# Kernel tuning notes

Hardware: AMD Instinct MI355X
Metric: run time of the kernel (lower is better)

The kernel has to match this reference:

```python
import jax, jax.numpy as jnp
import numpy as np

D_MODEL = 1024
N_HEADS = 16
HEAD_DIM = D_MODEL // N_HEADS


def setup_inputs() -> dict:
    key = jax.random.key(0)
    ks = jax.random.split(key, 5)
    B, S = 4, 2048
    scale = 1.0 / np.sqrt(D_MODEL)
    return {
        "x": jax.random.normal(ks[0], (B, S, D_MODEL), dtype=jnp.float32),
        "wq": jax.random.normal(ks[1], (D_MODEL, D_MODEL), dtype=jnp.float32) * scale,
        "wk": jax.random.normal(ks[2], (D_MODEL, D_MODEL), dtype=jnp.float32) * scale,
        "wv": jax.random.normal(ks[3], (D_MODEL, D_MODEL), dtype=jnp.float32) * scale,
        "wo": jax.random.normal(ks[4], (D_MODEL, D_MODEL), dtype=jnp.float32) * scale,
    }


def reference(x, wq, wk, wv, wo):
    B, S, _ = x.shape
    # projections: x @ W.T, then split heads -> [B, H, S, hd]
    def split_heads(t):
        return t.reshape(B, S, N_HEADS, HEAD_DIM).transpose(0, 2, 1, 3)

    q = split_heads(x @ wq.T)
    k = split_heads(x @ wk.T)
    v = split_heads(x @ wv.T)

    # scores [B, H, S, S], causal mask, stable softmax
    score = jnp.einsum("bhqd,bhkd->bhqk", q, k) / np.sqrt(HEAD_DIM)
    causal = jnp.tril(jnp.ones((S, S), dtype=bool))
    score = jnp.where(causal, score, -jnp.inf)
    attn = jax.nn.softmax(score, axis=-1)

    out = jnp.einsum("bhqk,bhkd->bhqd", attn, v)
    out = out.transpose(0, 2, 1, 3).reshape(B, S, D_MODEL)
    return out @ wo.T
```

## Files before the change

kernel.cpp:

```cpp
#include <hip/hip_runtime.h>
#include <type_traits>


typedef unsigned short u16;
typedef __attribute__((ext_vector_type(8))) short s8;
typedef __attribute__((ext_vector_type(4))) float f4;

__device__ __forceinline__ u16 f2bf(float f) {
    union { float f; unsigned u; } v; v.f = f;
    unsigned r = v.u + 0x7fffu + ((v.u >> 16) & 1u);
    return (u16)(r >> 16);
}

__device__ __forceinline__ unsigned pack_bf2(float a, float b) {
    return __builtin_amdgcn_perm(__float_as_uint(b), __float_as_uint(a),
                                 0x07060302u);
}

__device__ __forceinline__ void cp16(const void* g, void* l) {
    __builtin_amdgcn_global_load_lds(
        (const __attribute__((address_space(1))) unsigned int*)g,
        (__attribute__((address_space(3))) unsigned int*)l, 16, 0, 0);
}

__device__ __forceinline__ s8 load8f(const float* p) {
    const float4 lo = *(const float4*)p;
    const float4 hi = *(const float4*)(p + 4);
    s8 r;
    r[0] = (short)f2bf(lo.x); r[1] = (short)f2bf(lo.y);
    r[2] = (short)f2bf(lo.z); r[3] = (short)f2bf(lo.w);
    r[4] = (short)f2bf(hi.x); r[5] = (short)f2bf(hi.y);
    r[6] = (short)f2bf(hi.z); r[7] = (short)f2bf(hi.w);
    return r;
}

__global__ __launch_bounds__(256)
void f32_to_bf16(const float* __restrict__ in, u16* __restrict__ out, int n8)
{
    const int i = blockIdx.x * 256 + threadIdx.x;
    if (i < n8) *(s8*)(out + (size_t)i * 8) = load8f(in + (size_t)i * 8);
}

__global__ __launch_bounds__(256)
void cvt_w3(const float* __restrict__ a, const float* __restrict__ b2,
            const float* __restrict__ c3, u16* __restrict__ o, int per)
{
    const int y = blockIdx.y;
    const float* src = (y == 0) ? a : ((y == 1) ? b2 : c3);
    u16* dst = o + (size_t)y * per;
    const int i = blockIdx.x * 256 + threadIdx.x;
    *(s8*)(dst + (size_t)i * 8) = load8f(src + (size_t)i * 8);
}

template<typename TC>
__global__ __launch_bounds__(256)
void gemm_bb(const u16* __restrict__ A,
             const u16* __restrict__ W0, const u16* __restrict__ W1,
             const u16* __restrict__ W2,
             TC* __restrict__ C0, TC* __restrict__ C1,
             u16* __restrict__ VT, int K)
{
    __shared__ u16 As[128 * 32];
    __shared__ u16 Bs[128 * 32];

    const int t  = threadIdx.x;
    const int bm = blockIdx.x;
    const int nglob = blockIdx.y * 128;

    const u16* W; int nloc, mode;
    if (nglob < 1024)      { W = W0; nloc = nglob;        mode = 0; }
    else if (nglob < 2048) { W = W1; nloc = nglob - 1024; mode = 1; }
    else                   { W = W2; nloc = nglob - 2048; mode = 2; }

    const int lane = t & 63, w = t >> 6;
    const int wm = (w >> 1) * 64, wn = (w & 1) * 64;
    const int quad = lane >> 4, l16 = lane & 15;

    const int sc = (((lane & 3) ^ ((lane >> 3) & 3))) * 8;
    const int sr = w * 32 + (lane >> 2);
    const u16* Ag0 = A + (size_t)(bm * 128 + sr) * K + sc;
    const u16* Ag1 = Ag0 + (size_t)16 * K;
    const u16* Wg0 = W + (size_t)(nloc + sr) * K + sc;
    const u16* Wg1 = Wg0 + (size_t)16 * K;
    u16* Al0 = As + (w * 32) * 32;
    u16* Al1 = As + (w * 32 + 16) * 32;
    u16* Bl0 = Bs + (w * 32) * 32;
    u16* Bl1 = Bs + (w * 32 + 16) * 32;

    const int ca = (quad ^ ((l16 >> 1) & 3)) * 8;

    f4 acc[4][4];
    for (int i = 0; i < 4; i++)
        for (int j = 0; j < 4; j++)
            acc[i][j] = (f4){0.f, 0.f, 0.f, 0.f};

    for (int k0 = 0; k0 < K; k0 += 32) {
        __syncthreads();
        cp16(Ag0 + k0, Al0);
        cp16(Ag1 + k0, Al1);
        cp16(Wg0 + k0, Bl0);
        cp16(Wg1 + k0, Bl1);
        __syncthreads();

        s8 af[4], bf[4];
        for (int i = 0; i < 4; i++)
            af[i] = *(const s8*)&As[(wm + i * 16 + l16) * 32 + ca];
        for (int j = 0; j < 4; j++)
            bf[j] = *(const s8*)&Bs[(wn + j * 16 + l16) * 32 + ca];
        for (int i = 0; i < 4; i++)
            for (int j = 0; j < 4; j++)
                acc[i][j] = __builtin_amdgcn_mfma_f32_16x16x32_bf16(
                                af[i], bf[j], acc[i][j], 0, 0, 0);
    }

    if (mode == 2) {
        for (int i = 0; i < 4; i++) {
            const int row0 = bm * 128 + wm + i * 16 + quad * 4;
            const int b = row0 >> 11, s = row0 & 2047;
            for (int j = 0; j < 4; j++) {
                const int n = nloc + wn + j * 16 + l16;
                const int h = n >> 6, d = n & 63;
                unsigned lo = ((unsigned)f2bf(acc[i][j][1]) << 16) | f2bf(acc[i][j][0]);
                unsigned hi = ((unsigned)f2bf(acc[i][j][3]) << 16) | f2bf(acc[i][j][2]);
                *(uint2*)(VT + ((size_t)((b * 16 + h) * 64 + d)) * 2048 + s) =
                    make_uint2(lo, hi);
            }
        }
    } else {
        TC* C = (mode == 0) ? C0 : C1;
        for (int i = 0; i < 4; i++) {
            const int row = bm * 128 + wm + i * 16 + quad * 4;
            for (int j = 0; j < 4; j++) {
                const int col = nloc + wn + j * 16 + l16;
                for (int r = 0; r < 4; r++) {
                    if constexpr (std::is_same<TC, float>::value)
                        C[(size_t)(row + r) * 1024 + col] = acc[i][j][r];
                    else
                        C[(size_t)(row + r) * 1024 + col] = f2bf(acc[i][j][r]);
                }
            }
        }
    }
}

#define PSTR 72

__global__ __launch_bounds__(256)
void attn256(const u16* __restrict__ Q, const u16* __restrict__ K,
             const u16* __restrict__ Vt, u16* __restrict__ O)
{
    __shared__ u16 Ks[64 * 64];
    __shared__ u16 Vs[64 * 64];
    __shared__ u16 Ps[4][64 * PSTR];

    const int h  = blockIdx.x;
    const int b  = blockIdx.y;
    const int qb = 7 - blockIdx.z;

    const int t = threadIdx.x, lane = t & 63, w = t >> 6;
    const int quad = lane >> 4, l16 = lane & 15;
    const int colH = h * 64;
    const size_t rowQ0 = (size_t)b * 2048 + qb * 256 + w * 64;

    s8 qf[4][2];
    for (int i = 0; i < 4; i++)
        for (int kk = 0; kk < 2; kk++)
            qf[i][kk] = *(const s8*)&Q[(rowQ0 + i * 16 + l16) * 1024 +
                                       colH + kk * 32 + quad * 8];

    s8 ones;
    for (int e = 0; e < 8; e++) ones[e] = (short)0x3F80;

    f4 o_acc[4][4];
    f4 l_acc[4];
    for (int i = 0; i < 4; i++) {
        l_acc[i] = (f4){0.f, 0.f, 0.f, 0.f};
        for (int j = 0; j < 4; j++)
            o_acc[i][j] = (f4){0.f, 0.f, 0.f, 0.f};
    }

    const int ktmax_blk = qb * 4 + 4;
    const int ktmax_w   = qb * 4 + w + 1;

    const int vrow = lane >> 3;
    const int scc  = ((lane & 7) ^ vrow) * 8;
    const int r0   = w * 16 + vrow;
    const u16* Kg0 = K  + ((size_t)b * 2048 + r0) * 1024 + colH + scc;
    const u16* Kg1 = Kg0 + (size_t)8 * 1024;
    const u16* Vg0 = Vt + ((size_t)(b * 16 + h) * 64 + r0) * 2048 + scc;
    const u16* Vg1 = Vg0 + (size_t)8 * 2048;
    u16* Kl0 = Ks + (w * 16) * 64;      u16* Kl1 = Ks + (w * 16 + 8) * 64;
    u16* Vl0 = Vs + (w * 16) * 64;      u16* Vl1 = Vs + (w * 16 + 8) * 64;

    const float cexp = 0.18033688f;

    for (int kt = 0; kt < ktmax_blk; ++kt) {
        __syncthreads();
        cp16(Kg0 + (size_t)kt * 64 * 1024, Kl0);
        cp16(Kg1 + (size_t)kt * 64 * 1024, Kl1);
        cp16(Vg0 + kt * 64, Vl0);
        cp16(Vg1 + kt * 64, Vl1);
        __syncthreads();
        if (kt >= ktmax_w) continue;

        f4 sa[4][4];
        for (int j = 0; j < 4; j++)
            for (int i = 0; i < 4; i++)
                sa[j][i] = (f4){0.f, 0.f, 0.f, 0.f};
        for (int kk = 0; kk < 2; kk++) {
            s8 kf[4];
            for (int j = 0; j < 4; j++)
                kf[j] = *(const s8*)&Ks[(j * 16 + l16) * 64 +
                                        (((kk * 4 + quad) ^ (l16 & 7)) * 8)];
            for (int j = 0; j < 4; j++)
                for (int i = 0; i < 4; i++)
                    sa[j][i] = __builtin_amdgcn_mfma_f32_16x16x32_bf16(
                                   kf[j], qf[i][kk], sa[j][i], 0, 0, 0);
        }

        const bool diag = (kt == ktmax_w - 1);
        for (int i = 0; i < 4; i++) {
            const int q_l = i * 16 + l16;
            for (int j = 0; j < 4; j++) {
                const int kv0 = j * 16 + quad * 4;
                float p0 = exp2f(sa[j][i][0] * cexp);
                float p1 = exp2f(sa[j][i][1] * cexp);
                float p2 = exp2f(sa[j][i][2] * cexp);
                float p3 = exp2f(sa[j][i][3] * cexp);
                if (diag) {
                    if (kv0 + 0 > q_l) p0 = 0.f;
                    if (kv0 + 1 > q_l) p1 = 0.f;
                    if (kv0 + 2 > q_l) p2 = 0.f;
                    if (kv0 + 3 > q_l) p3 = 0.f;
                }
                *(uint2*)&Ps[w][q_l * PSTR + kv0] =
                    make_uint2(pack_bf2(p0, p1), pack_bf2(p2, p3));
            }
        }

        for (int kk = 0; kk < 2; kk++) {
            s8 pf[4], vf[4];
            for (int i = 0; i < 4; i++)
                pf[i] = *(const s8*)&Ps[w][(i * 16 + l16) * PSTR +
                                           kk * 32 + quad * 8];
            for (int jd = 0; jd < 4; jd++)
                vf[jd] = *(const s8*)&Vs[(jd * 16 + l16) * 64 +
                                         (((kk * 4 + quad) ^ (l16 & 7)) * 8)];
            for (int i = 0; i < 4; i++)
                l_acc[i] = __builtin_amdgcn_mfma_f32_16x16x32_bf16(
                               pf[i], ones, l_acc[i], 0, 0, 0);
            for (int i = 0; i < 4; i++)
                for (int jd = 0; jd < 4; jd++)
                    o_acc[i][jd] = __builtin_amdgcn_mfma_f32_16x16x32_bf16(
                                       pf[i], vf[jd], o_acc[i][jd], 0, 0, 0);
        }
    }

    for (int i = 0; i < 4; i++) {
        float rinv[4];
        for (int r = 0; r < 4; r++) rinv[r] = 1.0f / l_acc[i][r];
        for (int jd = 0; jd < 4; jd++)
            for (int r = 0; r < 4; r++) {
                const size_t row = rowQ0 + i * 16 + quad * 4 + r;
                O[row * 1024 + colH + jd * 16 + l16] =
                    f2bf(o_acc[i][jd][r] * rinv[r]);
            }
    }
}

extern "C" void kernel_launch(void* const* d_in, const int* in_sizes, int n_in,
                              void* d_out, int out_size, void* d_ws, size_t ws_size,
                              hipStream_t stream)
{
    const float* x  = (const float*)d_in[0];
    const float* wq = (const float*)d_in[1];
    const float* wk = (const float*)d_in[2];
    const float* wv = (const float*)d_in[3];
    const float* wo = (const float*)d_in[4];
    float* out = (float*)d_out;

    const size_t MD = (size_t)8192 * 1024;
    const size_t WD = (size_t)1024 * 1024;
    u16* Qb  = (u16*)d_ws;
    u16* Kb  = Qb + MD;
    u16* Vtb = Kb + MD;
    u16* Xb  = Vtb + MD;
    u16* Wqkv = (u16*)d_out;
    u16* Ob  = Qb;
    u16* Wob = Kb;

    f32_to_bf16<<<4096, 256, 0, stream>>>(x, Xb, (int)(MD / 8));

    cvt_w3<<<dim3(512, 3), 256, 0, stream>>>(wq, wk, wv, Wqkv, (int)WD);

    gemm_bb<u16><<<dim3(64, 24), 256, 0, stream>>>(
        Xb, Wqkv, Wqkv + WD, Wqkv + 2 * WD, Qb, Kb, Vtb, 1024);

    attn256<<<dim3(16, 4, 8), 256, 0, stream>>>(Qb, Kb, Vtb, Ob);

    f32_to_bf16<<<512, 256, 0, stream>>>(wo, Wob, (int)(WD / 8));

    gemm_bb<float><<<dim3(64, 8), 256, 0, stream>>>(
        Ob, Wob, Wob, Wob, out, out, nullptr, 1024);
}
```

Measured before the change: 296.4 us.

## Prefetch K/V tiles via registers, fold softmax scale into Q projection, remap query blocks

The attention kernel no longer loads K/V tiles straight into LDS with global_load_lds. It now prefetches the next tile into registers while the current tile is being computed, then stores those registers to LDS after the barrier. The softmax exp2 scale moves into the Q projection epilogue, which removes one multiply per score element. The query-block order is remapped so the heaviest causal blocks are spread differently across the grid. Risks are higher register pressure from the prefetch registers and a small precision change from rounding the pre-scaled Q to bf16.

New measurement: 296.8 us. About the same (+0.1%).

```diff
diff --git a/kernel.cpp b/kernel.cpp
--- a/kernel.cpp
+++ b/kernel.cpp
@@ -58,7 +58,7 @@
              const u16* __restrict__ W0, const u16* __restrict__ W1,
              const u16* __restrict__ W2,
              TC* __restrict__ C0, TC* __restrict__ C1,
-             u16* __restrict__ VT, int K)
+             u16* __restrict__ VT, int K, float cscale)
 {
     __shared__ u16 As[128 * 32];
     __shared__ u16 Bs[128 * 32];
@@ -128,15 +128,17 @@
         }
     } else {
         TC* C = (mode == 0) ? C0 : C1;
+        const float cs = (mode == 0) ? cscale : 1.0f;
         for (int i = 0; i < 4; i++) {
             const int row = bm * 128 + wm + i * 16 + quad * 4;
             for (int j = 0; j < 4; j++) {
                 const int col = nloc + wn + j * 16 + l16;
                 for (int r = 0; r < 4; r++) {
+                    const float val = acc[i][j][r] * cs;
                     if constexpr (std::is_same<TC, float>::value)
-                        C[(size_t)(row + r) * 1024 + col] = acc[i][j][r];
+                        C[(size_t)(row + r) * 1024 + col] = val;
                     else
-                        C[(size_t)(row + r) * 1024 + col] = f2bf(acc[i][j][r]);
+                        C[(size_t)(row + r) * 1024 + col] = f2bf(val);
                 }
             }
         }
@@ -155,7 +157,8 @@
 
     const int h  = blockIdx.x;
     const int b  = blockIdx.y;
-    const int qb = 7 - blockIdx.z;
+    const int QBMAP[8] = {7, 6, 5, 4, 0, 1, 2, 3};
+    const int qb = QBMAP[blockIdx.z];
 
     const int t = threadIdx.x, lane = t & 63, w = t >> 6;
     const int quad = lane >> 4, l16 = lane & 15;
@@ -189,70 +192,84 @@
     const u16* Kg1 = Kg0 + (size_t)8 * 1024;
     const u16* Vg0 = Vt + ((size_t)(b * 16 + h) * 64 + r0) * 2048 + scc;
     const u16* Vg1 = Vg0 + (size_t)8 * 2048;
-    u16* Kl0 = Ks + (w * 16) * 64;      u16* Kl1 = Ks + (w * 16 + 8) * 64;
-    u16* Vl0 = Vs + (w * 16) * 64;      u16* Vl1 = Vs + (w * 16 + 8) * 64;
-
-    const float cexp = 0.18033688f;
+    const int lds_off = (lane & 7) * 8;
+    u16* Kl0 = Ks + (w * 16 + vrow) * 64 + lds_off;
+    u16* Kl1 = Ks + (w * 16 + 8 + vrow) * 64 + lds_off;
+    u16* Vl0 = Vs + (w * 16 + vrow) * 64 + lds_off;
+    u16* Vl1 = Vs + (w * 16 + 8 + vrow) * 64 + lds_off;
+
+    s8 kr0 = *(const s8*)(Kg0);
+    s8 kr1 = *(const s8*)(Kg1);
+    s8 vr0 = *(const s8*)(Vg0);
+    s8 vr1 = *(const s8*)(Vg1);
 
     for (int kt = 0; kt < ktmax_blk; ++kt) {
         __syncthreads();
-        cp16(Kg0 + (size_t)kt * 64 * 1024, Kl0);
-        cp16(Kg1 + (size_t)kt * 64 * 1024, Kl1);
-        cp16(Vg0 + kt * 64, Vl0);
-        cp16(Vg1 + kt * 64, Vl1);
+        *(s8*)Kl0 = kr0;
+        *(s8*)Kl1 = kr1;
+        *(s8*)Vl0 = vr0;
+        *(s8*)Vl1 = vr1;
         __syncthreads();
-        if (kt >= ktmax_w) continue;
-
-        f4 sa[4][4];
-        for (int j = 0; j < 4; j++)
-            for (int i = 0; i < 4; i++)
-                sa[j][i] = (f4){0.f, 0.f, 0.f, 0.f};
-        for (int kk = 0; kk < 2; kk++) {
-            s8 kf[4];
-            for (int j = 0; j < 4; j++)
-                kf[j] = *(const s8*)&Ks[(j * 16 + l16) * 64 +
-                                        (((kk * 4 + quad) ^ (l16 & 7)) * 8)];
+
+        if (kt + 1 < ktmax_blk) {
+            kr0 = *(const s8*)(Kg0 + (size_t)(kt + 1) * 65536);
+            kr1 = *(const s8*)(Kg1 + (size_t)(kt + 1) * 65536);
+            vr0 = *(const s8*)(Vg0 + (kt + 1) * 64);
+            vr1 = *(const s8*)(Vg1 + (kt + 1) * 64);
+        }
+
+        if (kt < ktmax_w) {
+            f4 sa[4][4];
             for (int j = 0; j < 4; j++)
                 for (int i = 0; i < 4; i++)
-                    sa[j][i] = __builtin_amdgcn_mfma_f32_16x16x32_bf16(
-                                   kf[j], qf[i][kk], sa[j][i], 0, 0, 0);
-        }
-
-        const bool diag = (kt == ktmax_w - 1);
-        for (int i = 0; i < 4; i++) {
-            const int q_l = i * 16 + l16;
-            for (int j = 0; j < 4; j++) {
-                const int kv0 = j * 16 + quad * 4;
-                float p0 = exp2f(sa[j][i][0] * cexp);
-                float p1 = exp2f(sa[j][i][1] * cexp);
-                float p2 = exp2f(sa[j][i][2] * cexp);
-                float p3 = exp2f(sa[j][i][3] * cexp);
-                if (diag) {
-                    if (kv0 + 0 > q_l) p0 = 0.f;
-                    if (kv0 + 1 > q_l) p1 = 0.f;
-                    if (kv0 + 2 > q_l) p2 = 0.f;
-                    if (kv0 + 3 > q_l) p3 = 0.f;
+                    sa[j][i] = (f4){0.f, 0.f, 0.f, 0.f};
+            for (int kk = 0; kk < 2; kk++) {
+                s8 kf[4];
+                for (int j = 0; j < 4; j++)
+                    kf[j] = *(const s8*)&Ks[(j * 16 + l16) * 64 +
+                                            (((kk * 4 + quad) ^ (l16 & 7)) * 8)];
+                for (int j = 0; j < 4; j++)
+                    for (int i = 0; i < 4; i++)
+                        sa[j][i] = __builtin_amdgcn_mfma_f32_16x16x32_bf16(
+                                       kf[j], qf[i][kk], sa[j][i], 0, 0, 0);
+            }
+
+            const bool diag = (kt == ktmax_w - 1);
+            for (int i = 0; i < 4; i++) {
+                const int q_l = i * 16 + l16;
+                for (int j = 0; j < 4; j++) {
+                    const int kv0 = j * 16 + quad * 4;
+                    float p0 = exp2f(sa[j][i][0]);
+                    float p1 = exp2f(sa[j][i][1]);
+                    float p2 = exp2f(sa[j][i][2]);
+                    float p3 = exp2f(sa[j][i][3]);
+                    if (diag) {
+                        if (kv0 + 0 > q_l) p0 = 0.f;
+                        if (kv0 + 1 > q_l) p1 = 0.f;
+                        if (kv0 + 2 > q_l) p2 = 0.f;
+                        if (kv0 + 3 > q_l) p3 = 0.f;
+                    }
+                    *(uint2*)&Ps[w][q_l * PSTR + kv0] =
+                        make_uint2(pack_bf2(p0, p1), pack_bf2(p2, p3));
                 }
-                *(uint2*)&Ps[w][q_l * PSTR + kv0] =
-                    make_uint2(pack_bf2(p0, p1), pack_bf2(p2, p3));
-            }
-        }
-
-        for (int kk = 0; kk < 2; kk++) {
-            s8 pf[4], vf[4];
-            for (int i = 0; i < 4; i++)
-                pf[i] = *(const s8*)&Ps[w][(i * 16 + l16) * PSTR +
-                                           kk * 32 + quad * 8];
-            for (int jd = 0; jd < 4; jd++)
-                vf[jd] = *(const s8*)&Vs[(jd * 16 + l16) * 64 +
-                                         (((kk * 4 + quad) ^ (l16 & 7)) * 8)];
-            for (int i = 0; i < 4; i++)
-                l_acc[i] = __builtin_amdgcn_mfma_f32_16x16x32_bf16(
-                               pf[i], ones, l_acc[i], 0, 0, 0);
-            for (int i = 0; i < 4; i++)
+            }
+
+            for (int kk = 0; kk < 2; kk++) {
+                s8 pf[4], vf[4];
+                for (int i = 0; i < 4; i++)
+                    pf[i] = *(const s8*)&Ps[w][(i * 16 + l16) * PSTR +
+                                               kk * 32 + quad * 8];
                 for (int jd = 0; jd < 4; jd++)
-                    o_acc[i][jd] = __builtin_amdgcn_mfma_f32_16x16x32_bf16(
-                                       pf[i], vf[jd], o_acc[i][jd], 0, 0, 0);
+                    vf[jd] = *(const s8*)&Vs[(jd * 16 + l16) * 64 +
+                                             (((kk * 4 + quad) ^ (l16 & 7)) * 8)];
+                for (int i = 0; i < 4; i++)
+                    l_acc[i] = __builtin_amdgcn_mfma_f32_16x16x32_bf16(
+                                   pf[i], ones, l_acc[i], 0, 0, 0);
+                for (int i = 0; i < 4; i++)
+                    for (int jd = 0; jd < 4; jd++)
+                        o_acc[i][jd] = __builtin_amdgcn_mfma_f32_16x16x32_bf16(
+                                           pf[i], vf[jd], o_acc[i][jd], 0, 0, 0);
+            }
         }
     }
 
@@ -294,12 +311,12 @@
     cvt_w3<<<dim3(512, 3), 256, 0, stream>>>(wq, wk, wv, Wqkv, (int)WD);
 
     gemm_bb<u16><<<dim3(64, 24), 256, 0, stream>>>(
-        Xb, Wqkv, Wqkv + WD, Wqkv + 2 * WD, Qb, Kb, Vtb, 1024);
+        Xb, Wqkv, Wqkv + WD, Wqkv + 2 * WD, Qb, Kb, Vtb, 1024, 0.18033688f);
 
     attn256<<<dim3(16, 4, 8), 256, 0, stream>>>(Qb, Kb, Vtb, Ob);
 
     f32_to_bf16<<<512, 256, 0, stream>>>(wo, Wob, (int)(WD / 8));
 
     gemm_bb<float><<<dim3(64, 8), 256, 0, stream>>>(
-        Ob, Wob, Wob, Wob, out, out, nullptr, 1024);
-}
+        Ob, Wob, Wob, Wob, out, out, nullptr, 1024, 1.0f);
+}
```
